# Kernel optimization log

Measured on AMD Instinct MI355X. Metric: run time of the kernel, lower is better.

## Reference

```python
import math
import jax, jax.numpy as jnp
import numpy as np

B, S, DIM_OBS, DIM_ACT = 4, 512, 64, 8
D, NH, DH, FF, L = 1024, 16, 64, 4096, 6


def _ln(x, g, b, eps=1e-5):
    m = x.mean(-1, keepdims=True)
    v = ((x - m) ** 2).mean(-1, keepdims=True)
    return (x - m) / jnp.sqrt(v + eps) * g + b


def _pe(n, d):
    pos = jnp.arange(n, dtype=jnp.float32)[:, None]
    div = jnp.exp(jnp.arange(0, d, 2, dtype=jnp.float32) * (-math.log(10000.0) / d))
    pe = jnp.zeros((n, d), jnp.float32)
    pe = pe.at[:, 0::2].set(jnp.sin(pos * div))
    pe = pe.at[:, 1::2].set(jnp.cos(pos * div))
    return pe


def setup_inputs() -> dict:
    key = jax.random.key(0)
    ks = iter(jax.random.split(key, 40))
    n = lambda shape: jax.random.normal(next(ks), shape, jnp.float32) * 0.02
    return {
        "observations": jax.random.normal(next(ks), (B, S, DIM_OBS), jnp.float32),
        "actions": jax.random.normal(next(ks), (B, S, DIM_ACT), jnp.float32),
        "attn_mask": jnp.ones((B, S), jnp.bool_),
        "W_obs": n((D, DIM_OBS)), "b_obs": jnp.zeros((D,), jnp.float32),
        "W_act": n((D, DIM_ACT)), "b_act": jnp.zeros((D,), jnp.float32),
        "ln0_g": jnp.ones((D,), jnp.float32), "ln0_b": jnp.zeros((D,), jnp.float32),
        "Wq": n((L, D, D)), "Wk": n((L, D, D)), "Wv": n((L, D, D)),
        "Wo": n((L, D, D)), "bo": jnp.zeros((L, D), jnp.float32),
        "ln1_g": jnp.ones((L, D), jnp.float32), "ln1_b": jnp.zeros((L, D), jnp.float32),
        "Wf1": n((L, FF, D)), "bf1": jnp.zeros((L, FF), jnp.float32),
        "Wf2": n((L, D, FF)), "bf2": jnp.zeros((L, D), jnp.float32),
        "W_pred": n((DIM_ACT, S * D)), "b_pred": jnp.zeros((DIM_ACT,), jnp.float32),
    }


def reference(observations, actions, attn_mask, W_obs, b_obs, W_act, b_act,
              ln0_g, ln0_b, Wq, Wk, Wv, Wo, bo, ln1_g, ln1_b,
              Wf1, bf1, Wf2, bf2, W_pred, b_pred):
    b, s = observations.shape[:2]
    pe = _pe(s, D)
    obs_e = observations @ W_obs.T + b_obs + pe
    act_e = actions @ W_act.T + b_act + pe
    # interleave obs/act tokens -> (B, 2S, D)
    x = jnp.stack([obs_e, act_e], axis=2).reshape(b, 2 * s, D)
    x = _ln(x, ln0_g, ln0_b)
    m = ~attn_mask  # ones in -> all-False mask (no-op fill), matching original
    m2 = jnp.stack([m, m], axis=2).reshape(b, 2 * s)[:, None, None, :]
    scale = 1.0 / jnp.sqrt(jnp.float32(DH))

    def layer(h, p):
        wq, wk, wv, wo, bo_, g1, b1_, wf1, bf1_, wf2, bf2_ = p
        t = h.shape[1]
        q = (h @ wq.T).reshape(b, t, NH, DH)
        k = (h @ wk.T).reshape(b, t, NH, DH)
        v = (h @ wv.T).reshape(b, t, NH, DH)
        a = jnp.einsum('bqhd,bkhd->bhqk', q, k) * scale
        a = jnp.where(m2, -1e9, a)
        # FAITHFUL BUG: original multiplies unnormalized scores by V (softmax unused)
        av = jnp.einsum('bhqk,bkhd->bqhd', a, v).reshape(b, t, D)
        attn_out = av @ wo.T + bo_
        h1 = _ln(h + attn_out, g1, b1_)
        f = jax.nn.gelu(h1 @ wf1.T + bf1_, approximate=False)
        # FAITHFUL BUG: layer returns raw ffn output (no residual / ln2)
        return f @ wf2.T + bf2_, None

    x, _ = jax.lax.scan(layer, x, (Wq, Wk, Wv, Wo, bo, ln1_g, ln1_b, Wf1, bf1, Wf2, bf2))
    dec_act = x.reshape(b, s, 2, D)[:, :, 1, :].reshape(b, s * D)
    return jnp.tanh(dec_act @ W_pred.T + b_pred)
```

## Files before the change

kernel.cpp:

```cpp
#include <hip/hip_runtime.h>

typedef __attribute__((ext_vector_type(8))) _Float16 half8;
typedef __attribute__((ext_vector_type(4))) _Float16 half4v;
typedef __attribute__((ext_vector_type(4))) float f32x4;

__device__ __forceinline__ void gload16(const void* g, void* l) {
  __builtin_amdgcn_global_load_lds((__attribute__((address_space(1))) void*)(g),
                                   (__attribute__((address_space(3))) void*)(l), 16, 0, 0);
}

__global__ __launch_bounds__(256) void embed_kernel(
    const float* __restrict__ obs, const float* __restrict__ act,
    const float* __restrict__ W_obs, const float* __restrict__ b_obs,
    const float* __restrict__ W_act, const float* __restrict__ b_act,
    float* __restrict__ e) {
  const int row = blockIdx.x;
  const int b = row >> 10, t = row & 1023;
  const int pos = t >> 1;
  const bool is_act = t & 1;
  __shared__ float in_row[64];
  const int tid = threadIdx.x;
  if (!is_act) { if (tid < 64) in_row[tid] = obs[(size_t)(b * 512 + pos) * 64 + tid]; }
  else         { if (tid < 8)  in_row[tid] = act[(size_t)(b * 512 + pos) * 8 + tid]; }
  __syncthreads();
  for (int d = tid; d < 1024; d += 256) {
    float acc;
    if (!is_act) {
      acc = b_obs[d];
      const float* w = &W_obs[d * 64];
      #pragma unroll 8
      for (int c = 0; c < 64; ++c) acc += in_row[c] * w[c];
    } else {
      acc = b_act[d];
      const float* w = &W_act[d * 8];
      #pragma unroll
      for (int c = 0; c < 8; ++c) acc += in_row[c] * w[c];
    }
    const int j = d >> 1;
    const float dv = expf((float)(2 * j) * (-9.210340371976184f / 1024.0f));
    const float ang = (float)pos * dv;
    acc += (d & 1) ? cosf(ang) : sinf(ang);
    e[(size_t)row * 1024 + d] = acc;
  }
}

template<bool RES, bool WF32>
__global__ __launch_bounds__(256) void ln_kernel(
    const float* __restrict__ in, const float* __restrict__ res,
    const float* __restrict__ g, const float* __restrict__ bta,
    float* __restrict__ of, _Float16* __restrict__ ohh, _Float16* __restrict__ ohl) {
  const int row = blockIdx.x;
  const size_t base = (size_t)row * 1024;
  const int tid = threadIdx.x;
  float v[4];
  {
    const f32x4 a = *(const f32x4*)&in[base + tid * 4];
    if (RES) {
      const f32x4 r = *(const f32x4*)&res[base + tid * 4];
      v[0] = a[0] + r[0]; v[1] = a[1] + r[1]; v[2] = a[2] + r[2]; v[3] = a[3] + r[3];
    } else {
      v[0] = a[0]; v[1] = a[1]; v[2] = a[2]; v[3] = a[3];
    }
  }
  float s = 0.f, sq = 0.f;
  #pragma unroll
  for (int c = 0; c < 4; ++c) { s += v[c]; sq += v[c] * v[c]; }
  #pragma unroll
  for (int off = 32; off; off >>= 1) { s += __shfl_down(s, off); sq += __shfl_down(sq, off); }
  __shared__ float rs[4], rq[4];
  const int wid = tid >> 6, lane = tid & 63;
  if (!lane) { rs[wid] = s; rq[wid] = sq; }
  __syncthreads();
  s = rs[0] + rs[1] + rs[2] + rs[3];
  sq = rq[0] + rq[1] + rq[2] + rq[3];
  const float mean = s * (1.f / 1024.f);
  const float var = sq * (1.f / 1024.f) - mean * mean;
  const float rstd = rsqrtf(var + 1e-5f);
  #pragma unroll
  for (int c = 0; c < 4; ++c) {
    const int d = tid * 4 + c;
    const float o = (v[c] - mean) * rstd * g[d] + bta[d];
    if (WF32) of[base + d] = o;
    const _Float16 hi = (_Float16)o;
    ohh[base + d] = hi;
    ohl[base + d] = (_Float16)(o - (float)hi);
  }
}

__global__ __launch_bounds__(256) void f2h_split_kernel(const float* __restrict__ s,
                                                        _Float16* __restrict__ hi,
                                                        _Float16* __restrict__ lo, int n) {
  int i = (blockIdx.x * 256 + threadIdx.x) * 4;
  const int stride = gridDim.x * 256 * 4;
  for (; i < n; i += stride) {
    const f32x4 v = *(const f32x4*)&s[i];
    half4v h, l;
    #pragma unroll
    for (int c = 0; c < 4; ++c) {
      h[c] = (_Float16)v[c];
      l[c] = (_Float16)(v[c] - (float)h[c]);
    }
    *(half4v*)&hi[i] = h;
    *(half4v*)&lo[i] = l;
  }
}

template<bool BIAS, bool GELU, bool WF32, bool WF16>
__global__ __launch_bounds__(256, 2) void gemm_bt(
    const _Float16* __restrict__ Ah, const _Float16* __restrict__ Al,
    const _Float16* __restrict__ Bh, const _Float16* __restrict__ Bl,
    const float* __restrict__ bias,
    float* __restrict__ Cf, _Float16* __restrict__ Chh, _Float16* __restrict__ Chl,
    const int M, const int N, const int K) {
  __shared__ _Float16 lds[2][4][4096];
  const int tid = threadIdx.x;
  const int wid = tid >> 6, lane = tid & 63;
  const int wm = wid >> 1, wn = wid & 1;

  const int nwg = gridDim.x * gridDim.y;
  int flat = blockIdx.y * gridDim.x + blockIdx.x;
  flat = (flat & 7) * (nwg >> 3) + (flat >> 3);
  const int m0 = (flat / gridDim.x) * 128, n0 = (flat % gridDim.x) * 128;
  const int KT = K >> 5;

  f32x4 acc[4][4];
  #pragma unroll
  for (int i = 0; i < 4; ++i)
    #pragma unroll
    for (int j = 0; j < 4; ++j) acc[i][j] = f32x4{0.f, 0.f, 0.f, 0.f};

  const int ho0 = wid * 512 + lane * 8;
  const int r0s = ho0 >> 5, kk0 = ho0 & 31;
  const int ho1 = (wid + 4) * 512 + lane * 8;
  const int r1s = ho1 >> 5, kk1 = ho1 & 31;

  auto stage = [&](int buf, int kt) {
    const int k0 = kt << 5;
    const size_t a0 = (size_t)(m0 + r0s) * K + k0 + kk0;
    const size_t a1 = (size_t)(m0 + r1s) * K + k0 + kk1;
    const size_t b0 = (size_t)(n0 + r0s) * K + k0 + kk0;
    const size_t b1 = (size_t)(n0 + r1s) * K + k0 + kk1;
    gload16(Ah + a0, &lds[buf][0][ho0]); gload16(Ah + a1, &lds[buf][0][ho1]);
    gload16(Al + a0, &lds[buf][1][ho0]); gload16(Al + a1, &lds[buf][1][ho1]);
    gload16(Bh + b0, &lds[buf][2][ho0]); gload16(Bh + b1, &lds[buf][2][ho1]);
    gload16(Bl + b0, &lds[buf][3][ho0]); gload16(Bl + b1, &lds[buf][3][ho1]);
  };

  stage(0, 0);
  int cur = 0;
  const int lr = lane & 15, lk = (lane >> 4) * 8;
  for (int kt = 0; kt < KT; ++kt) {
    __syncthreads();
    if (kt + 1 < KT) stage(cur ^ 1, kt + 1);
    const _Float16* lAh = &lds[cur][0][0];
    const _Float16* lAl = &lds[cur][1][0];
    const _Float16* lBh = &lds[cur][2][0];
    const _Float16* lBl = &lds[cur][3][0];
    half8 afh[4], afl[4], bfh[4], bfl[4];
    #pragma unroll
    for (int mi = 0; mi < 4; ++mi) {
      const int o = (wm * 64 + mi * 16 + lr) * 32 + lk;
      afh[mi] = *(const half8*)&lAh[o];
      afl[mi] = *(const half8*)&lAl[o];
    }
    #pragma unroll
    for (int ni = 0; ni < 4; ++ni) {
      const int o = (wn * 64 + ni * 16 + lr) * 32 + lk;
      bfh[ni] = *(const half8*)&lBh[o];
      bfl[ni] = *(const half8*)&lBl[o];
    }
    #pragma unroll
    for (int mi = 0; mi < 4; ++mi)
      #pragma unroll
      for (int ni = 0; ni < 4; ++ni) {
        acc[mi][ni] = __builtin_amdgcn_mfma_f32_16x16x32_f16(afh[mi], bfh[ni], acc[mi][ni], 0, 0, 0);
        acc[mi][ni] = __builtin_amdgcn_mfma_f32_16x16x32_f16(afl[mi], bfh[ni], acc[mi][ni], 0, 0, 0);
        acc[mi][ni] = __builtin_amdgcn_mfma_f32_16x16x32_f16(afh[mi], bfl[ni], acc[mi][ni], 0, 0, 0);
      }
    cur ^= 1;
  }

  const int lq = lane >> 4;
  #pragma unroll
  for (int mi = 0; mi < 4; ++mi) {
    const int gr = m0 + wm * 64 + mi * 16 + lq * 4;
    #pragma unroll
    for (int ni = 0; ni < 4; ++ni) {
      const int gc = n0 + wn * 64 + ni * 16 + lr;
      float bv = 0.f;
      if (BIAS) bv = bias[gc];
      #pragma unroll
      for (int j = 0; j < 4; ++j) {
        float v = acc[mi][ni][j] + bv;
        if (GELU) v = 0.5f * v * (1.f + erff(v * 0.70710678118654752f));
        const size_t o = (size_t)(gr + j) * N + gc;
        if (WF32) Cf[o] = v;
        if (WF16) {
          const _Float16 hi = (_Float16)v;
          Chh[o] = hi;
          Chl[o] = (_Float16)(v - (float)hi);
        }
      }
    }
  }
}

__global__ __launch_bounds__(256) void ktv_kernel(const _Float16* __restrict__ qh,
                                                  const _Float16* __restrict__ ql,
                                                  float* __restrict__ Mp) {
  const int bid = blockIdx.x;
  const int q = bid & 3, bh = bid >> 2;
  const int b = bh >> 4, h = bh & 15;
  __shared__ float Ks[8192], Vs[8192];
  const int tid = threadIdx.x;
  const int tq = tid >> 6;
  const int tile = tid & 63;
  const int i0 = (tile >> 3) * 8, j0 = (tile & 7) * 8;
  float acc[8][8];
  #pragma unroll
  for (int ii = 0; ii < 8; ++ii)
    #pragma unroll
    for (int jj = 0; jj < 8; ++jj) acc[ii][jj] = 0.f;

  for (int cc = 0; cc < 2; ++cc) {
    const int c = q * 2 + cc;
    for (int idx = tid * 8; idx < 8192; idx += 2048) {
      const int r = idx >> 6, kk = idx & 63;
      const size_t g = (size_t)(b * 1024 + c * 128 + r) * 3072 + h * 64 + kk;
      const half8 k_h = *(const half8*)&qh[g + 1024];
      const half8 k_l = *(const half8*)&ql[g + 1024];
      const half8 v_h = *(const half8*)&qh[g + 2048];
      const half8 v_l = *(const half8*)&ql[g + 2048];
      #pragma unroll
      for (int xx = 0; xx < 8; ++xx) {
        Ks[idx + xx] = (float)k_h[xx] + (float)k_l[xx];
        Vs[idx + xx] = (float)v_h[xx] + (float)v_l[xx];
      }
    }
    __syncthreads();
    for (int r = tq * 32; r < tq * 32 + 32; ++r) {
      float kv[8], vv[8];
      #pragma unroll
      for (int xx = 0; xx < 8; ++xx) { kv[xx] = Ks[r * 64 + i0 + xx]; vv[xx] = Vs[r * 64 + j0 + xx]; }
      #pragma unroll
      for (int ii = 0; ii < 8; ++ii)
        #pragma unroll
        for (int jj = 0; jj < 8; ++jj) acc[ii][jj] += kv[ii] * vv[jj];
    }
    __syncthreads();
  }
  __shared__ float red[64][64];
  for (int pp = 0; pp < 4; ++pp) {
    if (tq == pp) {
      #pragma unroll
      for (int ii = 0; ii < 8; ++ii)
        #pragma unroll
        for (int jj = 0; jj < 8; ++jj) {
          if (pp == 0) red[tile][ii * 8 + jj] = acc[ii][jj];
          else         red[tile][ii * 8 + jj] += acc[ii][jj];
        }
    }
    __syncthreads();
  }
  for (int o = tid; o < 4096; o += 256) {
    const int i = o >> 6, j = o & 63;
    Mp[((size_t)(q * 64 + bh) << 12) + o] = red[(i >> 3) * 8 + (j >> 3)][(i & 7) * 8 + (j & 7)];
  }
}

__global__ __launch_bounds__(256) void av_kernel(const _Float16* __restrict__ qh,
                                                 const _Float16* __restrict__ ql,
                                                 const float* __restrict__ Mp,
                                                 _Float16* __restrict__ avh,
                                                 _Float16* __restrict__ avl) {
  const int id = blockIdx.x;
  const int tc = id & 7, bh = id >> 3;
  const int b = bh >> 4, h = bh & 15;
  __shared__ float Ms[4096];
  __shared__ float Qs[8192];
  const int tid = threadIdx.x;
  for (int o = tid * 4; o < 4096; o += 1024) {
    const f32x4 p0 = *(const f32x4*)&Mp[((size_t)(bh) << 12) + o];
    const f32x4 p1 = *(const f32x4*)&Mp[((size_t)(64 + bh) << 12) + o];
    const f32x4 p2 = *(const f32x4*)&Mp[((size_t)(128 + bh) << 12) + o];
    const f32x4 p3 = *(const f32x4*)&Mp[((size_t)(192 + bh) << 12) + o];
    f32x4 m;
    #pragma unroll
    for (int c = 0; c < 4; ++c) m[c] = 0.125f * (p0[c] + p1[c] + p2[c] + p3[c]);
    *(f32x4*)&Ms[o] = m;
  }
  for (int idx = tid * 8; idx < 8192; idx += 2048) {
    const int r = idx >> 6, kk = idx & 63;
    const size_t g = (size_t)(b * 1024 + tc * 128 + r) * 3072 + h * 64 + kk;
    const half8 q_h = *(const half8*)&qh[g];
    const half8 q_l = *(const half8*)&ql[g];
    #pragma unroll
    for (int xx = 0; xx < 8; ++xx) Qs[idx + xx] = (float)q_h[xx] + (float)q_l[xx];
  }
  __syncthreads();
  const int r0 = (tid >> 3) * 4, j0 = (tid & 7) * 8;
  float acc[4][8];
  #pragma unroll
  for (int rr = 0; rr < 4; ++rr)
    #pragma unroll
    for (int jj = 0; jj < 8; ++jj) acc[rr][jj] = 0.f;
  for (int i = 0; i < 64; ++i) {
    float m8[8];
    #pragma unroll
    for (int jj = 0; jj < 8; ++jj) m8[jj] = Ms[i * 64 + j0 + jj];
    #pragma unroll
    for (int rr = 0; rr < 4; ++rr) {
      const float qv = Qs[(r0 + rr) * 64 + i];
      #pragma unroll
      for (int jj = 0; jj < 8; ++jj) acc[rr][jj] += qv * m8[jj];
    }
  }
  #pragma unroll
  for (int rr = 0; rr < 4; ++rr)
    #pragma unroll
    for (int jj = 0; jj < 8; ++jj) {
      const size_t o = (size_t)(b * 1024 + tc * 128 + r0 + rr) * 1024 + h * 64 + j0 + jj;
      const float v = acc[rr][jj];
      const _Float16 hi = (_Float16)v;
      avh[o] = hi;
      avl[o] = (_Float16)(v - (float)hi);
    }
}

__global__ __launch_bounds__(256) void pred_split1(const float* __restrict__ x,
                                                   const float* __restrict__ Wp,
                                                   float* __restrict__ partial) {
  const int bid = blockIdx.x;
  const int b = bid >> 9, a = (bid >> 6) & 7, sp = bid & 63;
  const int tid = threadIdx.x;
  const int base = sp * 8192;
  float acc = 0.f;
  #pragma unroll
  for (int it = 0; it < 8; ++it) {
    const int i4 = base + it * 1024 + tid * 4;
    const int s = i4 >> 10, d = i4 & 1023;
    const f32x4 xv = *(const f32x4*)&x[(size_t)(b * 1024 + 2 * s + 1) * 1024 + d];
    const f32x4 wv = *(const f32x4*)&Wp[(size_t)a * 524288 + i4];
    acc += xv[0] * wv[0] + xv[1] * wv[1] + xv[2] * wv[2] + xv[3] * wv[3];
  }
  #pragma unroll
  for (int off = 32; off; off >>= 1) acc += __shfl_down(acc, off);
  __shared__ float red[4];
  const int wid = tid >> 6, lane = tid & 63;
  if (!lane) red[wid] = acc;
  __syncthreads();
  if (tid == 0) partial[bid] = red[0] + red[1] + red[2] + red[3];
}

__global__ __launch_bounds__(64) void pred_split2(const float* __restrict__ partial,
                                                  const float* __restrict__ bp,
                                                  float* __restrict__ out) {
  const int pair = blockIdx.x;
  const int lane = threadIdx.x;
  float v = partial[pair * 64 + lane];
  #pragma unroll
  for (int off = 32; off; off >>= 1) v += __shfl_down(v, off);
  if (lane == 0) out[pair] = tanhf(v + bp[pair & 7]);
}

extern "C" void kernel_launch(void* const* d_in, const int* in_sizes, int n_in,
                              void* d_out, int out_size, void* d_ws, size_t ws_size,
                              hipStream_t stream) {
  (void)in_sizes; (void)n_in; (void)out_size; (void)ws_size;
  const float* obs    = (const float*)d_in[0];
  const float* act    = (const float*)d_in[1];
  const float* W_obs  = (const float*)d_in[3];
  const float* b_obs  = (const float*)d_in[4];
  const float* W_act  = (const float*)d_in[5];
  const float* b_act  = (const float*)d_in[6];
  const float* ln0_g  = (const float*)d_in[7];
  const float* ln0_b  = (const float*)d_in[8];
  const float* Wq     = (const float*)d_in[9];
  const float* Wk     = (const float*)d_in[10];
  const float* Wv     = (const float*)d_in[11];
  const float* Wo     = (const float*)d_in[12];
  const float* bo     = (const float*)d_in[13];
  const float* ln1_g  = (const float*)d_in[14];
  const float* ln1_b  = (const float*)d_in[15];
  const float* Wf1    = (const float*)d_in[16];
  const float* bf1    = (const float*)d_in[17];
  const float* Wf2    = (const float*)d_in[18];
  const float* bf2    = (const float*)d_in[19];
  const float* W_pred = (const float*)d_in[20];
  const float* b_pred = (const float*)d_in[21];
  float* out = (float*)d_out;

  char* p = (char*)d_ws;
  auto alloc = [&](size_t bytes) { char* r = p; p += (bytes + 255) & ~(size_t)255; return r; };
  const size_t MB = 1024 * 1024;
  _Float16* whqkv_h = (_Float16*)alloc(6 * MB);
  _Float16* whqkv_l = (_Float16*)alloc(6 * MB);
  _Float16* who_h   = (_Float16*)alloc(2 * MB);
  _Float16* who_l   = (_Float16*)alloc(2 * MB);
  _Float16* whf1_h  = (_Float16*)alloc(8 * MB);
  _Float16* whf1_l  = (_Float16*)alloc(8 * MB);
  _Float16* whf2_h  = (_Float16*)alloc(8 * MB);
  _Float16* whf2_l  = (_Float16*)alloc(8 * MB);
  float*    e       = (float*)alloc(16 * MB);
  float*    x       = (float*)alloc(16 * MB);
  _Float16* xh_h    = (_Float16*)alloc(8 * MB);
  _Float16* xh_l    = (_Float16*)alloc(8 * MB);
  _Float16* av_h    = (_Float16*)alloc(8 * MB);
  _Float16* av_l    = (_Float16*)alloc(8 * MB);
  _Float16* h1_h    = (_Float16*)alloc(8 * MB);
  _Float16* h1_l    = (_Float16*)alloc(8 * MB);
  float*    Mp      = (float*)alloc(4 * MB);
  float*    pred_p  = (float*)alloc(2048 * 4);
  char*     U       = alloc(64 * MB);
  _Float16* qkv_h = (_Float16*)U;
  _Float16* qkv_l = (_Float16*)(U + 24 * MB);
  _Float16* fh_h  = (_Float16*)U;
  _Float16* fh_l  = (_Float16*)(U + 32 * MB);
  float* ao = e;

  auto f2h = [&](const float* s, _Float16* hh, _Float16* ll, int n) {
    int blocks = (n / 4 + 255) / 256; if (blocks > 2048) blocks = 2048;
    f2h_split_kernel<<<blocks, 256, 0, stream>>>(s, hh, ll, n);
  };

  embed_kernel<<<4096, 256, 0, stream>>>(obs, act, W_obs, b_obs, W_act, b_act, e);
  ln_kernel<false, true><<<4096, 256, 0, stream>>>(e, nullptr, ln0_g, ln0_b, x, xh_h, xh_l);

  for (int l = 0; l < 6; ++l) {
    const size_t dd = (size_t)l * 1024 * 1024, df = (size_t)l * 4096 * 1024;
    f2h(Wq + dd, whqkv_h,           whqkv_l,           1048576);
    f2h(Wk + dd, whqkv_h + 1048576, whqkv_l + 1048576, 1048576);
    f2h(Wv + dd, whqkv_h + 2097152, whqkv_l + 2097152, 1048576);
    f2h(Wo + dd, who_h,  who_l,  1048576);
    f2h(Wf1 + df, whf1_h, whf1_l, 4194304);
    f2h(Wf2 + df, whf2_h, whf2_l, 4194304);

    gemm_bt<false, false, false, true><<<dim3(24, 32), 256, 0, stream>>>(
        xh_h, xh_l, whqkv_h, whqkv_l, nullptr, nullptr, qkv_h, qkv_l, 4096, 3072, 1024);
    ktv_kernel<<<256, 256, 0, stream>>>(qkv_h, qkv_l, Mp);
    av_kernel<<<512, 256, 0, stream>>>(qkv_h, qkv_l, Mp, av_h, av_l);
    gemm_bt<true, false, true, false><<<dim3(8, 32), 256, 0, stream>>>(
        av_h, av_l, who_h, who_l, bo + (size_t)l * 1024, ao, nullptr, nullptr, 4096, 1024, 1024);
    ln_kernel<true, false><<<4096, 256, 0, stream>>>(
        x, ao, ln1_g + (size_t)l * 1024, ln1_b + (size_t)l * 1024, nullptr, h1_h, h1_l);
    gemm_bt<true, true, false, true><<<dim3(32, 32), 256, 0, stream>>>(
        h1_h, h1_l, whf1_h, whf1_l, bf1 + (size_t)l * 4096, nullptr, fh_h, fh_l, 4096, 4096, 1024);
    gemm_bt<true, false, true, true><<<dim3(8, 32), 256, 0, stream>>>(
        fh_h, fh_l, whf2_h, whf2_l, bf2 + (size_t)l * 1024, x, xh_h, xh_l, 4096, 1024, 4096);
  }

  pred_split1<<<2048, 256, 0, stream>>>(x, W_pred, pred_p);
  pred_split2<<<32, 64, 0, stream>>>(pred_p, b_pred, out);
}
```

Measured before the change: 2.731 ms.

## Add 256x256-tile split-fp16 GEMM with staggered prefetch for QKV and FF1

Adds a new 512-thread GEMM kernel that computes 256x256 output tiles, with 8 waves each holding 128x64 of accumulators. It loads the hi and lo fp16 operand parts in separate phases, interleaving the next tile's prefetch with the three MFMA passes (hi*hi, lo*hi, hi*lo). It also raises wave priority around the MFMA blocks. The QKV and FF1 projections now use it, aiming to cut LDS and global traffic per flop and to overlap loads with compute better. The costs are higher register pressure and 64 KB of LDS per block, which may limit occupancy, plus fewer blocks (192 or 256) on a GPU with many CUs, which risks tail imbalance.

```diff
diff --git a/kernel.cpp b/kernel.cpp
--- a/kernel.cpp
+++ b/kernel.cpp
@@ -116,7 +116,6 @@
   const int tid = threadIdx.x;
   const int wid = tid >> 6, lane = tid & 63;
   const int wm = wid >> 1, wn = wid & 1;
-
   const int nwg = gridDim.x * gridDim.y;
   int flat = blockIdx.y * gridDim.x + blockIdx.x;
   flat = (flat & 7) * (nwg >> 3) + (flat >> 3);
@@ -200,6 +199,146 @@
           Chh[o] = hi;
           Chl[o] = (_Float16)(v - (float)hi);
         }
+      }
+    }
+  }
+}
+
+template<bool BIAS, bool GELU>
+__global__ __launch_bounds__(512, 2) void gemm256(
+    const _Float16* __restrict__ Ah, const _Float16* __restrict__ Al,
+    const _Float16* __restrict__ Bh, const _Float16* __restrict__ Bl,
+    const float* __restrict__ bias,
+    _Float16* __restrict__ Chh, _Float16* __restrict__ Chl,
+    const int N, const int K) {
+  __shared__ _Float16 lds[2][4][8192];
+  const int tid = threadIdx.x;
+  const int wid = tid >> 6, lane = tid & 63;
+  const int wm = wid >> 2, wn = wid & 3;
+  const int nwg = gridDim.x * gridDim.y;
+  int flat = blockIdx.y * gridDim.x + blockIdx.x;
+  flat = (flat & 7) * (nwg >> 3) + (flat >> 3);
+  const int m0 = (flat / gridDim.x) * 256, n0 = (flat % gridDim.x) * 256;
+  const int KT = K >> 5;
+  const int lr = lane & 15, rch = lane >> 4;
+
+  int aoff[8], boff[4];
+  #pragma unroll
+  for (int m = 0; m < 8; ++m) {
+    const int row = wm * 128 + m * 16 + lr;
+    aoff[m] = row * 32 + ((rch ^ ((row >> 1) & 3)) << 3);
+  }
+  #pragma unroll
+  for (int n = 0; n < 4; ++n) {
+    const int row = wn * 64 + n * 16 + lr;
+    boff[n] = row * 32 + ((rch ^ ((row >> 1) & 3)) << 3);
+  }
+  int soff[2]; size_t sA[2], sB[2];
+  #pragma unroll
+  for (int j = 0; j < 2; ++j) {
+    const int ci = j * 512 + wid * 64 + lane;
+    const int row = ci >> 2;
+    const int cs = (((ci & 3) ^ ((row >> 1) & 3)) << 3);
+    soff[j] = ci * 8;
+    sA[j] = (size_t)(m0 + row) * K + cs;
+    sB[j] = (size_t)(n0 + row) * K + cs;
+  }
+
+  f32x4 acc[8][4];
+  #pragma unroll
+  for (int m = 0; m < 8; ++m)
+    #pragma unroll
+    for (int n = 0; n < 4; ++n) acc[m][n] = f32x4{0.f, 0.f, 0.f, 0.f};
+
+  auto stH = [&](int nb, int kt) {
+    const int k0 = kt << 5;
+    gload16(Ah + sA[0] + k0, &lds[nb][0][soff[0]]);
+    gload16(Ah + sA[1] + k0, &lds[nb][0][soff[1]]);
+    gload16(Bh + sB[0] + k0, &lds[nb][2][soff[0]]);
+    gload16(Bh + sB[1] + k0, &lds[nb][2][soff[1]]);
+  };
+  auto stAl = [&](int nb, int kt) {
+    const int k0 = kt << 5;
+    gload16(Al + sA[0] + k0, &lds[nb][1][soff[0]]);
+    gload16(Al + sA[1] + k0, &lds[nb][1][soff[1]]);
+  };
+  auto stBl = [&](int nb, int kt) {
+    const int k0 = kt << 5;
+    gload16(Bl + sB[0] + k0, &lds[nb][3][soff[0]]);
+    gload16(Bl + sB[1] + k0, &lds[nb][3][soff[1]]);
+  };
+
+  stH(0, 0); stAl(0, 0); stBl(0, 0);
+
+  for (int t = 0; t < KT; ++t) {
+    const int buf = t & 1, nb = buf ^ 1;
+    const bool pf = (t + 1 < KT);
+    asm volatile("s_waitcnt vmcnt(4)" ::: "memory");
+    __builtin_amdgcn_s_barrier();
+    __builtin_amdgcn_sched_barrier(0);
+    half8 ah[8], bh8[4], al[8], bl8[4];
+    #pragma unroll
+    for (int m = 0; m < 8; ++m) ah[m] = *(const half8*)&lds[buf][0][aoff[m]];
+    #pragma unroll
+    for (int n = 0; n < 4; ++n) bh8[n] = *(const half8*)&lds[buf][2][boff[n]];
+    if (pf) stH(nb, t + 1);
+    asm volatile("s_waitcnt lgkmcnt(0)" ::: "memory");
+    __builtin_amdgcn_sched_barrier(0);
+    __builtin_amdgcn_s_setprio(1);
+    #pragma unroll
+    for (int m = 0; m < 8; ++m)
+      #pragma unroll
+      for (int n = 0; n < 4; ++n)
+        acc[m][n] = __builtin_amdgcn_mfma_f32_16x16x32_f16(ah[m], bh8[n], acc[m][n], 0, 0, 0);
+    __builtin_amdgcn_s_setprio(0);
+    if (pf) { asm volatile("s_waitcnt vmcnt(4)" ::: "memory"); }
+    else    { asm volatile("s_waitcnt vmcnt(0)" ::: "memory"); }
+    __builtin_amdgcn_s_barrier();
+    __builtin_amdgcn_sched_barrier(0);
+    #pragma unroll
+    for (int m = 0; m < 8; ++m) al[m] = *(const half8*)&lds[buf][1][aoff[m]];
+    if (pf) stAl(nb, t + 1);
+    asm volatile("s_waitcnt lgkmcnt(0)" ::: "memory");
+    __builtin_amdgcn_sched_barrier(0);
+    __builtin_amdgcn_s_setprio(1);
+    #pragma unroll
+    for (int m = 0; m < 8; ++m)
+      #pragma unroll
+      for (int n = 0; n < 4; ++n)
+        acc[m][n] = __builtin_amdgcn_mfma_f32_16x16x32_f16(al[m], bh8[n], acc[m][n], 0, 0, 0);
+    __builtin_amdgcn_s_setprio(0);
+    #pragma unroll
+    for (int n = 0; n < 4; ++n) bl8[n] = *(const half8*)&lds[buf][3][boff[n]];
+    if (pf) stBl(nb, t + 1);
+    asm volatile("s_waitcnt lgkmcnt(0)" ::: "memory");
+    __builtin_amdgcn_sched_barrier(0);
+    __builtin_amdgcn_s_setprio(1);
+    #pragma unroll
+    for (int m = 0; m < 8; ++m)
+      #pragma unroll
+      for (int n = 0; n < 4; ++n)
+        acc[m][n] = __builtin_amdgcn_mfma_f32_16x16x32_f16(ah[m], bl8[n], acc[m][n], 0, 0, 0);
+    __builtin_amdgcn_s_setprio(0);
+    __builtin_amdgcn_s_barrier();
+  }
+
+  const int lq = lane >> 4;
+  #pragma unroll
+  for (int m = 0; m < 8; ++m) {
+    const int gr = m0 + wm * 128 + m * 16 + lq * 4;
+    #pragma unroll
+    for (int n = 0; n < 4; ++n) {
+      const int gc = n0 + wn * 64 + n * 16 + lr;
+      float bv = 0.f;
+      if (BIAS) bv = bias[gc];
+      #pragma unroll
+      for (int j = 0; j < 4; ++j) {
+        float v = acc[m][n][j] + bv;
+        if (GELU) v = 0.5f * v * (1.f + erff(v * 0.70710678118654752f));
+        const size_t o = (size_t)(gr + j) * N + gc;
+        const _Float16 hi = (_Float16)v;
+        Chh[o] = hi;
+        Chl[o] = (_Float16)(v - (float)hi);
       }
     }
   }
@@ -435,16 +574,16 @@
     f2h(Wf1 + df, whf1_h, whf1_l, 4194304);
     f2h(Wf2 + df, whf2_h, whf2_l, 4194304);
 
-    gemm_bt<false, false, false, true><<<dim3(24, 32), 256, 0, stream>>>(
-        xh_h, xh_l, whqkv_h, whqkv_l, nullptr, nullptr, qkv_h, qkv_l, 4096, 3072, 1024);
+    gemm256<false, false><<<dim3(12, 16), 512, 0, stream>>>(
+        xh_h, xh_l, whqkv_h, whqkv_l, nullptr, qkv_h, qkv_l, 3072, 1024);
     ktv_kernel<<<256, 256, 0, stream>>>(qkv_h, qkv_l, Mp);
     av_kernel<<<512, 256, 0, stream>>>(qkv_h, qkv_l, Mp, av_h, av_l);
     gemm_bt<true, false, true, false><<<dim3(8, 32), 256, 0, stream>>>(
         av_h, av_l, who_h, who_l, bo + (size_t)l * 1024, ao, nullptr, nullptr, 4096, 1024, 1024);
     ln_kernel<true, false><<<4096, 256, 0, stream>>>(
         x, ao, ln1_g + (size_t)l * 1024, ln1_b + (size_t)l * 1024, nullptr, h1_h, h1_l);
-    gemm_bt<true, true, false, true><<<dim3(32, 32), 256, 0, stream>>>(
-        h1_h, h1_l, whf1_h, whf1_l, bf1 + (size_t)l * 4096, nullptr, fh_h, fh_l, 4096, 4096, 1024);
+    gemm256<true, true><<<dim3(16, 16), 512, 0, stream>>>(
+        h1_h, h1_l, whf1_h, whf1_l, bf1 + (size_t)l * 4096, fh_h, fh_l, 4096, 1024);
     gemm_bt<true, false, true, true><<<dim3(8, 32), 256, 0, stream>>>(
         fh_h, fh_l, whf2_h, whf2_l, bf2 + (size_t)l * 1024, x, xh_h, xh_l, 4096, 1024, 4096);
   }
```

Result: faster. 2.607 ms (-4.5%).
